# Kernel optimization log

Hardware: AMD Instinct MI355X
Metric: run time of the kernel (lower is better)

The kernel has to match this reference:

```python
import jax, jax.numpy as jnp
import numpy as np
import math

B, S, D = 16, 4096, 64

def setup_inputs() -> dict:
    key = jax.random.key(0)
    kq, kk, kv = jax.random.split(key, 3)
    query = jax.random.normal(kq, (B, S, D), dtype=jnp.float32)
    k_ = jax.random.normal(kk, (B, S, D), dtype=jnp.float32)
    value = jax.random.normal(kv, (B, S, D), dtype=jnp.float32)
    # causal mask: 1 = allowed, 0 = masked (set to -inf), broadcast over batch
    mask = jnp.tril(jnp.ones((S, S), dtype=jnp.int32))[None, :, :]
    return {"query": query, "key": k_, "value": value, "mask": mask, "key_dim": D}

def reference(query, key, value, mask, key_dim):
    # scores: [B, S, S] = Q @ K^T / sqrt(dk)
    scores = jnp.einsum('bqd,bkd->bqk', query, key) / math.sqrt(key_dim)
    scores = jnp.where(mask == 0, -jnp.inf, scores)
    attn = jax.nn.softmax(scores, axis=-1)
    return jnp.einsum('bqk,bkd->bqd', attn, value)
```

## Files before the change

kernel.cpp:

```cpp
#include <hip/hip_runtime.h>

typedef _Float16 half8 __attribute__((ext_vector_type(8)));
typedef float f32x4 __attribute__((ext_vector_type(4)));

union Frag {
    half8 v;
    unsigned int u32[4];
    uint4 u4;
};

constexpr int S = 4096;
constexpr int D = 64;
constexpr int B = 16;
constexpr int LTS = 72;

__global__ __launch_bounds__(256)
void convert_f16_kernel(const float* __restrict__ in, _Float16* __restrict__ out, int n8) {
    int i = blockIdx.x * 256 + threadIdx.x;
    if (i >= n8) return;
    float4 a = ((const float4*)in)[2 * i];
    float4 c = ((const float4*)in)[2 * i + 1];
    Frag f;
    f.v[0] = (_Float16)a.x; f.v[1] = (_Float16)a.y;
    f.v[2] = (_Float16)a.z; f.v[3] = (_Float16)a.w;
    f.v[4] = (_Float16)c.x; f.v[5] = (_Float16)c.y;
    f.v[6] = (_Float16)c.z; f.v[7] = (_Float16)c.w;
    ((uint4*)out)[i] = f.u4;
}

__global__ __launch_bounds__(256)
void transpose_v_kernel(const float* __restrict__ V, _Float16* __restrict__ VT) {
    __shared__ float tl[64 * 68];
    const int tid = threadIdx.x;
    const int s0 = blockIdx.x * 64;
    const int b = blockIdx.y;
    const float* Vb = V + (size_t)b * S * D;
    #pragma unroll
    for (int i = 0; i < 4; ++i) {
        int fi = tid + 256 * i;
        int r = fi >> 4, c4 = (fi & 15) << 2;
        float4 v = *(const float4*)(Vb + (size_t)(s0 + r) * D + c4);
        *(float4*)(&tl[r * 68 + c4]) = v;
    }
    __syncthreads();
    _Float16* VTb = VT + (size_t)b * D * S;
    #pragma unroll
    for (int i = 0; i < 2; ++i) {
        int fi = tid + 256 * i;
        int d = fi >> 3, s8 = (fi & 7) << 3;
        Frag f;
        #pragma unroll
        for (int j = 0; j < 8; ++j) f.v[j] = (_Float16)tl[(s8 + j) * 68 + d];
        *(uint4*)(VTb + (size_t)d * S + s0 + s8) = f.u4;
    }
}

__global__ __launch_bounds__(256, 4)
void fattn_kernel(const float* __restrict__ Q, const _Float16* __restrict__ K16,
                  const _Float16* __restrict__ VT16, float* __restrict__ Out) {
    __shared__ __align__(16) _Float16 kt[64 * LTS];
    __shared__ __align__(16) _Float16 vt[64 * LTS];
    __shared__ __align__(16) _Float16 pt[4 * 16 * LTS];

    const int tid = threadIdx.x;
    const int wave = tid >> 6;
    const int lane = tid & 63;
    const int ln = lane & 15;
    const int quad = lane >> 4;

    const int bx = blockIdx.x;
    const int b = bx & 15;
    const int qt = 63 - (bx >> 4);

    const float* Qb = Q + (size_t)b * S * D;
    const _Float16* Kb = K16 + (size_t)b * S * D;
    const _Float16* VTb = VT16 + (size_t)b * D * S;
    float* Ob = Out + (size_t)b * S * D;

    const float qscale = 0.125f * 1.44269504088896340736f;
    const int qrow_base = qt * 64 + wave * 16;

    Frag qf[2];
    {
        const float* qrow = Qb + (size_t)(qrow_base + ln) * D + quad * 8;
        #pragma unroll
        for (int ks = 0; ks < 2; ++ks) {
            float4 a = *(const float4*)(qrow + ks * 32);
            float4 c = *(const float4*)(qrow + ks * 32 + 4);
            Frag f;
            f.v[0] = (_Float16)(a.x * qscale); f.v[1] = (_Float16)(a.y * qscale);
            f.v[2] = (_Float16)(a.z * qscale); f.v[3] = (_Float16)(a.w * qscale);
            f.v[4] = (_Float16)(c.x * qscale); f.v[5] = (_Float16)(c.y * qscale);
            f.v[6] = (_Float16)(c.z * qscale); f.v[7] = (_Float16)(c.w * qscale);
            qf[ks] = f;
        }
    }

    f32x4 o[4] = {};
    float l_r[4] = {0.f, 0.f, 0.f, 0.f};
    _Float16* ptw = pt + wave * 16 * LTS;

    for (int t = 0; t <= qt; ++t) {
        const int k0 = t * 64;
        __syncthreads();

        #pragma unroll
        for (int i = 0; i < 2; ++i) {
            int fi = tid + 256 * i;
            int r = fi >> 3;
            int c8 = (fi & 7) << 3;
            uint4 kk = *(const uint4*)(Kb + (size_t)(k0 + r) * D + c8);
            uint4 vv = *(const uint4*)(VTb + (size_t)r * S + k0 + c8);
            *(uint4*)(kt + r * LTS + c8) = kk;
            *(uint4*)(vt + r * LTS + c8) = vv;
        }
        __syncthreads();

        f32x4 s[4];
        #pragma unroll
        for (int ct = 0; ct < 4; ++ct) {
            f32x4 acc = {0.f, 0.f, 0.f, 0.f};
            #pragma unroll
            for (int ks = 0; ks < 2; ++ks) {
                Frag kf;
                kf.u4 = *(const uint4*)(kt + (ct * 16 + ln) * LTS + ks * 32 + quad * 8);
                acc = __builtin_amdgcn_mfma_f32_16x16x32_f16(qf[ks].v, kf.v, acc, 0, 0, 0);
            }
            s[ct] = acc;
        }

        if (t == qt) {
            #pragma unroll
            for (int ct = 0; ct < 4; ++ct) {
                int kcol = k0 + ct * 16 + ln;
                #pragma unroll
                for (int r = 0; r < 4; ++r) {
                    int qrow = qrow_base + quad * 4 + r;
                    if (kcol > qrow) s[ct][r] = -1e30f;
                }
            }
        }

        #pragma unroll
        for (int ct = 0; ct < 4; ++ct) {
            #pragma unroll
            for (int r = 0; r < 4; ++r) {
                float p = exp2f(s[ct][r]);
                s[ct][r] = p;
                l_r[r] += p;
            }
        }

        #pragma unroll
        for (int r = 0; r < 4; ++r) {
            #pragma unroll
            for (int ct = 0; ct < 4; ++ct) {
                ptw[(quad * 4 + r) * LTS + ct * 16 + ln] = (_Float16)s[ct][r];
            }
        }
        Frag pf[2];
        #pragma unroll
        for (int ks = 0; ks < 2; ++ks) {
            pf[ks].u4 = *(const uint4*)(ptw + ln * LTS + ks * 32 + quad * 8);
        }

        #pragma unroll
        for (int sub = 0; sub < 4; ++sub) {
            #pragma unroll
            for (int ks = 0; ks < 2; ++ks) {
                Frag vf;
                vf.u4 = *(const uint4*)(vt + (sub * 16 + ln) * LTS + ks * 32 + quad * 8);
                o[sub] = __builtin_amdgcn_mfma_f32_16x16x32_f16(pf[ks].v, vf.v, o[sub], 0, 0, 0);
            }
        }
    }

    #pragma unroll
    for (int r = 0; r < 4; ++r) {
        float lt = l_r[r];
        #pragma unroll
        for (int off = 1; off <= 8; off <<= 1)
            lt += __shfl_xor(lt, off, 64);
        float inv = 1.0f / lt;
        #pragma unroll
        for (int sub = 0; sub < 4; ++sub) o[sub][r] *= inv;
    }
    #pragma unroll
    for (int sub = 0; sub < 4; ++sub) {
        #pragma unroll
        for (int r = 0; r < 4; ++r) {
            Ob[(size_t)(qrow_base + quad * 4 + r) * D + sub * 16 + ln] = o[sub][r];
        }
    }
}

extern "C" void kernel_launch(void* const* d_in, const int* in_sizes, int n_in,
                              void* d_out, int out_size, void* d_ws, size_t ws_size,
                              hipStream_t stream) {
    const float* Q = (const float*)d_in[0];
    const float* K = (const float*)d_in[1];
    const float* V = (const float*)d_in[2];
    float* O = (float*)d_out;

    _Float16* K16 = (_Float16*)d_ws;
    _Float16* VT16 = (_Float16*)((char*)d_ws + (size_t)B * S * D * 2);

    int n8 = B * S * D / 8;
    hipLaunchKernelGGL(convert_f16_kernel, dim3((n8 + 255) / 256), dim3(256), 0, stream, K, K16, n8);
    hipLaunchKernelGGL(transpose_v_kernel, dim3(S / 64, B), dim3(256), 0, stream, V, VT16);
    hipLaunchKernelGGL(fattn_kernel, dim3(64 * B), dim3(256), 0, stream, Q, K16, VT16, O);
}
```

Measured before the change: 213.1 us.

## Double query rows per block, compute S^T directly, fuse K/V prep kernels

Each block now handles 128 query rows, with 32 per wave in two 16-row groups. This halves the grid and lets every K/V tile loaded into LDS be reused across twice as many queries. The QK MFMA operands are swapped so each lane holds four consecutive keys for one query row, letting P be written to LDS as packed 4-half stores instead of scalar stores. Waves skip tiles beyond their own causal boundary. The K conversion and V transpose are merged into one prep kernel, and its LDS padding changes from 68 to 66. Trade-offs: the grid drops to 512 blocks, which may underfill the GPU, and the waves within a block do uneven work.

```diff
diff --git a/kernel.cpp b/kernel.cpp
--- a/kernel.cpp
+++ b/kernel.cpp
@@ -3,44 +3,43 @@
 typedef _Float16 half8 __attribute__((ext_vector_type(8)));
 typedef float f32x4 __attribute__((ext_vector_type(4)));
 
-union Frag {
-    half8 v;
-    unsigned int u32[4];
-    uint4 u4;
-};
+union Frag { half8 v; unsigned int u32[4]; uint4 u4; };
+union Pack4 { _Float16 h[4]; uint2 u; };
 
 constexpr int S = 4096;
 constexpr int D = 64;
-constexpr int B = 16;
+constexpr int NB = 16;
 constexpr int LTS = 72;
 
 __global__ __launch_bounds__(256)
-void convert_f16_kernel(const float* __restrict__ in, _Float16* __restrict__ out, int n8) {
-    int i = blockIdx.x * 256 + threadIdx.x;
-    if (i >= n8) return;
-    float4 a = ((const float4*)in)[2 * i];
-    float4 c = ((const float4*)in)[2 * i + 1];
-    Frag f;
-    f.v[0] = (_Float16)a.x; f.v[1] = (_Float16)a.y;
-    f.v[2] = (_Float16)a.z; f.v[3] = (_Float16)a.w;
-    f.v[4] = (_Float16)c.x; f.v[5] = (_Float16)c.y;
-    f.v[6] = (_Float16)c.z; f.v[7] = (_Float16)c.w;
-    ((uint4*)out)[i] = f.u4;
-}
-
-__global__ __launch_bounds__(256)
-void transpose_v_kernel(const float* __restrict__ V, _Float16* __restrict__ VT) {
-    __shared__ float tl[64 * 68];
+void prep_kernel(const float* __restrict__ K, const float* __restrict__ V,
+                 _Float16* __restrict__ K16, _Float16* __restrict__ VT) {
+    __shared__ float tl[64 * 66];
     const int tid = threadIdx.x;
     const int s0 = blockIdx.x * 64;
-    const int b = blockIdx.y;
-    const float* Vb = V + (size_t)b * S * D;
+    const int b  = blockIdx.y;
+    const float* Kb = K + ((size_t)b * S + s0) * D;
+    const float* Vb = V + ((size_t)b * S + s0) * D;
+    _Float16* K16b = K16 + ((size_t)b * S + s0) * D;
+
+    #pragma unroll
+    for (int i = 0; i < 2; ++i) {
+        int e8 = tid + 256 * i;
+        float4 a = ((const float4*)Kb)[2 * e8];
+        float4 c = ((const float4*)Kb)[2 * e8 + 1];
+        Frag f;
+        f.v[0]=(_Float16)a.x; f.v[1]=(_Float16)a.y; f.v[2]=(_Float16)a.z; f.v[3]=(_Float16)a.w;
+        f.v[4]=(_Float16)c.x; f.v[5]=(_Float16)c.y; f.v[6]=(_Float16)c.z; f.v[7]=(_Float16)c.w;
+        ((uint4*)K16b)[e8] = f.u4;
+    }
     #pragma unroll
     for (int i = 0; i < 4; ++i) {
         int fi = tid + 256 * i;
         int r = fi >> 4, c4 = (fi & 15) << 2;
-        float4 v = *(const float4*)(Vb + (size_t)(s0 + r) * D + c4);
-        *(float4*)(&tl[r * 68 + c4]) = v;
+        float4 v = *(const float4*)(Vb + (size_t)r * D + c4);
+        float2* p = (float2*)&tl[r * 66 + c4];
+        p[0] = make_float2(v.x, v.y);
+        p[1] = make_float2(v.z, v.w);
     }
     __syncthreads();
     _Float16* VTb = VT + (size_t)b * D * S;
@@ -50,7 +49,7 @@
         int d = fi >> 3, s8 = (fi & 7) << 3;
         Frag f;
         #pragma unroll
-        for (int j = 0; j < 8; ++j) f.v[j] = (_Float16)tl[(s8 + j) * 68 + d];
+        for (int j = 0; j < 8; ++j) f.v[j] = (_Float16)tl[(s8 + j) * 66 + d];
         *(uint4*)(VTb + (size_t)d * S + s0 + s8) = f.u4;
     }
 }
@@ -60,17 +59,17 @@
                   const _Float16* __restrict__ VT16, float* __restrict__ Out) {
     __shared__ __align__(16) _Float16 kt[64 * LTS];
     __shared__ __align__(16) _Float16 vt[64 * LTS];
-    __shared__ __align__(16) _Float16 pt[4 * 16 * LTS];
-
-    const int tid = threadIdx.x;
+    __shared__ __align__(16) _Float16 pt[4 * 32 * LTS];
+
+    const int tid  = threadIdx.x;
     const int wave = tid >> 6;
     const int lane = tid & 63;
-    const int ln = lane & 15;
+    const int ln   = lane & 15;
     const int quad = lane >> 4;
 
     const int bx = blockIdx.x;
-    const int b = bx & 15;
-    const int qt = 63 - (bx >> 4);
+    const int b  = bx & 15;
+    const int qt = 31 - (bx >> 4);
 
     const float* Qb = Q + (size_t)b * S * D;
     const _Float16* Kb = K16 + (size_t)b * S * D;
@@ -78,37 +77,39 @@
     float* Ob = Out + (size_t)b * S * D;
 
     const float qscale = 0.125f * 1.44269504088896340736f;
-    const int qrow_base = qt * 64 + wave * 16;
-
-    Frag qf[2];
-    {
-        const float* qrow = Qb + (size_t)(qrow_base + ln) * D + quad * 8;
+    const int qrow_base = qt * 128 + wave * 32;
+    const int tw = (qrow_base + 31) >> 6;
+    const int ntiles = 2 * qt + 2;
+
+    Frag qf[2][2];
+    #pragma unroll
+    for (int qg = 0; qg < 2; ++qg) {
+        const float* qrow = Qb + (size_t)(qrow_base + qg * 16 + ln) * D + quad * 8;
         #pragma unroll
         for (int ks = 0; ks < 2; ++ks) {
             float4 a = *(const float4*)(qrow + ks * 32);
             float4 c = *(const float4*)(qrow + ks * 32 + 4);
             Frag f;
-            f.v[0] = (_Float16)(a.x * qscale); f.v[1] = (_Float16)(a.y * qscale);
-            f.v[2] = (_Float16)(a.z * qscale); f.v[3] = (_Float16)(a.w * qscale);
-            f.v[4] = (_Float16)(c.x * qscale); f.v[5] = (_Float16)(c.y * qscale);
-            f.v[6] = (_Float16)(c.z * qscale); f.v[7] = (_Float16)(c.w * qscale);
-            qf[ks] = f;
-        }
-    }
-
-    f32x4 o[4] = {};
-    float l_r[4] = {0.f, 0.f, 0.f, 0.f};
-    _Float16* ptw = pt + wave * 16 * LTS;
-
-    for (int t = 0; t <= qt; ++t) {
+            f.v[0]=(_Float16)(a.x*qscale); f.v[1]=(_Float16)(a.y*qscale);
+            f.v[2]=(_Float16)(a.z*qscale); f.v[3]=(_Float16)(a.w*qscale);
+            f.v[4]=(_Float16)(c.x*qscale); f.v[5]=(_Float16)(c.y*qscale);
+            f.v[6]=(_Float16)(c.z*qscale); f.v[7]=(_Float16)(c.w*qscale);
+            qf[qg][ks] = f;
+        }
+    }
+
+    f32x4 o[2][4] = {};
+    float l_acc[2] = {0.f, 0.f};
+    _Float16* ptw = pt + wave * 32 * LTS;
+
+    for (int t = 0; t < ntiles; ++t) {
         const int k0 = t * 64;
         __syncthreads();
 
         #pragma unroll
         for (int i = 0; i < 2; ++i) {
             int fi = tid + 256 * i;
-            int r = fi >> 3;
-            int c8 = (fi & 7) << 3;
+            int r = fi >> 3, c8 = (fi & 7) << 3;
             uint4 kk = *(const uint4*)(Kb + (size_t)(k0 + r) * D + c8);
             uint4 vv = *(const uint4*)(VTb + (size_t)r * S + k0 + c8);
             *(uint4*)(kt + r * LTS + c8) = kk;
@@ -116,80 +117,72 @@
         }
         __syncthreads();
 
-        f32x4 s[4];
-        #pragma unroll
-        for (int ct = 0; ct < 4; ++ct) {
-            f32x4 acc = {0.f, 0.f, 0.f, 0.f};
-            #pragma unroll
-            for (int ks = 0; ks < 2; ++ks) {
-                Frag kf;
-                kf.u4 = *(const uint4*)(kt + (ct * 16 + ln) * LTS + ks * 32 + quad * 8);
-                acc = __builtin_amdgcn_mfma_f32_16x16x32_f16(qf[ks].v, kf.v, acc, 0, 0, 0);
-            }
-            s[ct] = acc;
-        }
-
-        if (t == qt) {
+        if (t <= tw) {
             #pragma unroll
             for (int ct = 0; ct < 4; ++ct) {
-                int kcol = k0 + ct * 16 + ln;
+                Frag kf0, kf1;
+                kf0.u4 = *(const uint4*)(kt + (ct * 16 + ln) * LTS + quad * 8);
+                kf1.u4 = *(const uint4*)(kt + (ct * 16 + ln) * LTS + 32 + quad * 8);
                 #pragma unroll
-                for (int r = 0; r < 4; ++r) {
-                    int qrow = qrow_base + quad * 4 + r;
-                    if (kcol > qrow) s[ct][r] = -1e30f;
+                for (int qg = 0; qg < 2; ++qg) {
+                    f32x4 acc = {0.f, 0.f, 0.f, 0.f};
+                    acc = __builtin_amdgcn_mfma_f32_16x16x32_f16(kf0.v, qf[qg][0].v, acc, 0, 0, 0);
+                    acc = __builtin_amdgcn_mfma_f32_16x16x32_f16(kf1.v, qf[qg][1].v, acc, 0, 0, 0);
+                    if (t == tw) {
+                        int keyb = k0 + ct * 16 + quad * 4;
+                        int qrow = qrow_base + qg * 16 + ln;
+                        #pragma unroll
+                        for (int r = 0; r < 4; ++r)
+                            if (keyb + r > qrow) acc[r] = -1e30f;
+                    }
+                    Pack4 pk;
+                    float psum = 0.f;
+                    #pragma unroll
+                    for (int r = 0; r < 4; ++r) {
+                        float p = exp2f(acc[r]);
+                        psum += p;
+                        pk.h[r] = (_Float16)p;
+                    }
+                    l_acc[qg] += psum;
+                    *(uint2*)(ptw + (qg * 16 + ln) * LTS + ct * 16 + quad * 4) = pk.u;
                 }
             }
-        }
-
-        #pragma unroll
-        for (int ct = 0; ct < 4; ++ct) {
-            #pragma unroll
-            for (int r = 0; r < 4; ++r) {
-                float p = exp2f(s[ct][r]);
-                s[ct][r] = p;
-                l_r[r] += p;
+
+            Frag pf[2][2];
+            #pragma unroll
+            for (int qg = 0; qg < 2; ++qg)
+                #pragma unroll
+                for (int ks = 0; ks < 2; ++ks)
+                    pf[qg][ks].u4 = *(const uint4*)(ptw + (qg * 16 + ln) * LTS + ks * 32 + quad * 8);
+
+            #pragma unroll
+            for (int ks = 0; ks < 2; ++ks) {
+                #pragma unroll
+                for (int sub = 0; sub < 4; ++sub) {
+                    Frag vf;
+                    vf.u4 = *(const uint4*)(vt + (sub * 16 + ln) * LTS + ks * 32 + quad * 8);
+                    #pragma unroll
+                    for (int qg = 0; qg < 2; ++qg)
+                        o[qg][sub] = __builtin_amdgcn_mfma_f32_16x16x32_f16(pf[qg][ks].v, vf.v, o[qg][sub], 0, 0, 0);
+                }
             }
         }
-
+    }
+
+    #pragma unroll
+    for (int qg = 0; qg < 2; ++qg) {
+        float lf = l_acc[qg];
+        lf += __shfl_xor(lf, 16, 64);
+        lf += __shfl_xor(lf, 32, 64);
         #pragma unroll
         for (int r = 0; r < 4; ++r) {
-            #pragma unroll
-            for (int ct = 0; ct < 4; ++ct) {
-                ptw[(quad * 4 + r) * LTS + ct * 16 + ln] = (_Float16)s[ct][r];
+            float lrow = __shfl(lf, quad * 4 + r, 64);
+            float inv = 1.0f / lrow;
+            #pragma unroll
+            for (int sub = 0; sub < 4; ++sub) {
+                Ob[(size_t)(qrow_base + qg * 16 + quad * 4 + r) * D + sub * 16 + ln] =
+                    o[qg][sub][r] * inv;
             }
-        }
-        Frag pf[2];
-        #pragma unroll
-        for (int ks = 0; ks < 2; ++ks) {
-            pf[ks].u4 = *(const uint4*)(ptw + ln * LTS + ks * 32 + quad * 8);
-        }
-
-        #pragma unroll
-        for (int sub = 0; sub < 4; ++sub) {
-            #pragma unroll
-            for (int ks = 0; ks < 2; ++ks) {
-                Frag vf;
-                vf.u4 = *(const uint4*)(vt + (sub * 16 + ln) * LTS + ks * 32 + quad * 8);
-                o[sub] = __builtin_amdgcn_mfma_f32_16x16x32_f16(pf[ks].v, vf.v, o[sub], 0, 0, 0);
-            }
-        }
-    }
-
-    #pragma unroll
-    for (int r = 0; r < 4; ++r) {
-        float lt = l_r[r];
-        #pragma unroll
-        for (int off = 1; off <= 8; off <<= 1)
-            lt += __shfl_xor(lt, off, 64);
-        float inv = 1.0f / lt;
-        #pragma unroll
-        for (int sub = 0; sub < 4; ++sub) o[sub][r] *= inv;
-    }
-    #pragma unroll
-    for (int sub = 0; sub < 4; ++sub) {
-        #pragma unroll
-        for (int r = 0; r < 4; ++r) {
-            Ob[(size_t)(qrow_base + quad * 4 + r) * D + sub * 16 + ln] = o[sub][r];
         }
     }
 }
@@ -203,10 +196,8 @@
     float* O = (float*)d_out;
 
     _Float16* K16 = (_Float16*)d_ws;
-    _Float16* VT16 = (_Float16*)((char*)d_ws + (size_t)B * S * D * 2);
-
-    int n8 = B * S * D / 8;
-    hipLaunchKernelGGL(convert_f16_kernel, dim3((n8 + 255) / 256), dim3(256), 0, stream, K, K16, n8);
-    hipLaunchKernelGGL(transpose_v_kernel, dim3(S / 64, B), dim3(256), 0, stream, V, VT16);
-    hipLaunchKernelGGL(fattn_kernel, dim3(64 * B), dim3(256), 0, stream, Q, K16, VT16, O);
+    _Float16* VT16 = (_Float16*)((char*)d_ws + (size_t)NB * S * D * 2);
+
+    hipLaunchKernelGGL(prep_kernel, dim3(S / 64, NB), dim3(256), 0, stream, K, V, K16, VT16);
+    hipLaunchKernelGGL(fattn_kernel, dim3(32 * NB), dim3(256), 0, stream, Q, K16, VT16, O);
 }
```

Measured after the change: 247.5 us. 1.16x slower.
